# Kernel optimization log

Measured on AMD Instinct MI355X. Metric: run time of the kernel, lower is better.

Reference implementation:

```python
import jax, jax.numpy as jnp
import numpy as np

N_NODES = 50000
N_EDGES = 600000
N_GRAPHS = 64
D_NODE = 64
D_EDGE = 16
HID = 128
N_LAYERS = 3
LN_EPS = 1e-5


def setup_inputs() -> dict:
    key = jax.random.key(0)
    ks = jax.random.split(key, 16)
    inp = {
        'x': jax.random.normal(ks[0], (N_NODES, D_NODE), dtype=jnp.float32),
        'edge_index': jax.random.randint(ks[1], (2, N_EDGES), 0, N_NODES, dtype=jnp.int64),
        'edge_attr': jax.random.normal(ks[2], (N_EDGES, D_EDGE), dtype=jnp.float32),
        'batch': jnp.sort(jax.random.randint(ks[3], (N_NODES,), 0, N_GRAPHS, dtype=jnp.int64)),
    }
    def lin(k, fan_in, fan_out):
        bound = 1.0 / np.sqrt(fan_in)
        kw, kb = jax.random.split(k)
        w = jax.random.uniform(kw, (fan_in, fan_out), minval=-bound, maxval=bound, dtype=jnp.float32)
        b = jax.random.uniform(kb, (fan_out,), minval=-bound, maxval=bound, dtype=jnp.float32)
        return w, b
    inp['enc_w'], inp['enc_b'] = lin(ks[4], D_NODE, HID)
    inp['ln_g'] = jnp.ones((HID,), jnp.float32)
    inp['ln_b'] = jnp.zeros((HID,), jnp.float32)
    inp['edge_w'], inp['edge_b'] = lin(ks[5], D_EDGE, HID // 2)
    cw, cb = [], []
    for i in range(N_LAYERS):
        w, b = lin(ks[6 + i], HID, HID)
        cw.append(w); cb.append(b)
    inp['conv_ws'] = jnp.stack(cw)  # [L, HID, HID]
    inp['conv_bs'] = jnp.stack(cb)  # [L, HID]
    inp['c1_w'], inp['c1_b'] = lin(ks[10], HID, HID // 2)
    inp['c2_w'], inp['c2_b'] = lin(ks[11], HID // 2, 1)
    return inp


def _layernorm(h, g, b):
    mu = jnp.mean(h, axis=-1, keepdims=True)
    var = jnp.mean(jnp.square(h - mu), axis=-1, keepdims=True)
    return (h - mu) * jax.lax.rsqrt(var + LN_EPS) * g + b


def _gcn_forward(x, edge_attr, batch, src, dst,
                 enc_w, enc_b, ln_g, ln_b, edge_w, edge_b,
                 conv_ws, conv_bs, c1_w, c1_b, c2_w, c2_b):
    # node encoder: Linear -> ReLU -> LayerNorm
    h = _layernorm(jax.nn.relu(x @ enc_w + enc_b), ln_g, ln_b)
    # edge encoder (output unused downstream, kept for fidelity)
    _ = jax.nn.relu(edge_attr @ edge_w + edge_b)
    # GCN normalization with self-loops: deg = in-degree + 1
    deg = jax.ops.segment_sum(jnp.ones((src.shape[0],), h.dtype), dst, num_segments=N_NODES) + 1.0
    dis = jax.lax.rsqrt(deg)  # deg >= 1
    edge_norm = (dis[src] * dis[dst])[:, None]
    self_norm = (dis * dis)[:, None]  # 1/deg for self-loop
    for i in range(N_LAYERS):
        hw = h @ conv_ws[i]
        agg = jax.ops.segment_sum(hw[src] * edge_norm, dst, num_segments=N_NODES)
        h = agg + hw * self_norm + conv_bs[i]
        h = jax.nn.relu(h)  # dropout is identity at eval
    # global mean pool over graphs
    sums = jax.ops.segment_sum(h, batch, num_segments=N_GRAPHS)
    cnts = jax.ops.segment_sum(jnp.ones((h.shape[0],), h.dtype), batch, num_segments=N_GRAPHS)
    pooled = sums / jnp.maximum(cnts, 1.0)[:, None]
    # classifier: Linear -> ReLU -> (Dropout) -> Linear
    return jax.nn.relu(pooled @ c1_w + c1_b) @ c2_w + c2_b


def reference(x, edge_index, edge_attr, batch, enc_w, enc_b, ln_g, ln_b,
              edge_w, edge_b, conv_ws, conv_bs, c1_w, c1_b, c2_w, c2_b):
    src, dst = edge_index[0], edge_index[1]
    return _gcn_forward(x, edge_attr, batch, src, dst, enc_w, enc_b, ln_g, ln_b,
                        edge_w, edge_b, conv_ws, conv_bs, c1_w, c1_b, c2_w, c2_b)
```

## Files before the change

### kernel.cpp

```cpp
#include <hip/hip_runtime.h>

#define HID 128
#define DNODE 64
#define NNODES 50000
#define NEDGES 600000
#define NGRAPHS 64
#define LN_EPS 1e-5f
#define SCAN_BLK 256
#define NSCAN ((NNODES + SCAN_BLK - 1) / SCAN_BLK)

#define NZERO (NNODES + NGRAPHS * HID)
#define NZERO4 (NZERO / 4)
#define Z_BLKS ((NZERO4 + 255) / 256)
#define PKWC_BLKS (3 * 16384 / 256)
#define PKWE_BLKS (8192 / 256)

#define ENC_BLKS ((NNODES + 63) / 64)
#define CNT_BLKS ((NEDGES + 255) / 256)
#define BND_BLKS ((NNODES + 255) / 256)

#define CONV_BLKS ((NNODES + 63) / 64)
#define FILL_BLKS ((NEDGES + 255) / 256)

#define GC_BLKS (NNODES / 16)

typedef __attribute__((ext_vector_type(8))) short bf16x8;
typedef __attribute__((ext_vector_type(8))) unsigned short u16x8;
typedef __attribute__((ext_vector_type(4))) float f32x4;

static __device__ __forceinline__ unsigned short f2bf(float f) {
  unsigned int u = __float_as_uint(f);
  u += 0x7fffu + ((u >> 16) & 1u);
  return (unsigned short)(u >> 16);
}
static __device__ __forceinline__ float bf2f(unsigned short h) {
  return __uint_as_float(((unsigned int)h) << 16);
}

__global__ void __launch_bounds__(256) prep0_kernel(
    int4* __restrict__ zp, const float* __restrict__ W,
    unsigned short* __restrict__ Wp, const float* __restrict__ enc_w,
    unsigned short* __restrict__ Wpe) {
  int b = blockIdx.x;
  if (b < Z_BLKS) {
    int i = b * 256 + threadIdx.x;
    if (i < NZERO4) zp[i] = make_int4(0, 0, 0, 0);
  } else if (b < Z_BLKS + PKWC_BLKS) {
    int t = (b - Z_BLKS) * 256 + threadIdx.x;
    int i = t & 7;
    int lane = (t >> 3) & 63;
    int kk = (t >> 9) & 3;
    int nt = (t >> 11) & 7;
    int layer = t >> 14;
    int k = kk * 32 + (lane >> 4) * 8 + i;
    int n = nt * 16 + (lane & 15);
    Wp[t] = f2bf(W[((size_t)layer * HID + k) * HID + n]);
  } else {
    int t = (b - Z_BLKS - PKWC_BLKS) * 256 + threadIdx.x;
    int i = t & 7;
    int lane = (t >> 3) & 63;
    int kk = (t >> 9) & 1;
    int nt = (t >> 10) & 7;
    int k = kk * 32 + (lane >> 4) * 8 + i;
    int n = nt * 16 + (lane & 15);
    Wpe[t] = f2bf(enc_w[(size_t)k * HID + n]);
  }
}

__global__ void __launch_bounds__(256) prep1_kernel(
    const float* __restrict__ x, const unsigned short* __restrict__ Wpe,
    const float* __restrict__ enc_b, const float* __restrict__ ln_g,
    const float* __restrict__ ln_b, unsigned short* __restrict__ Abf,
    const int* __restrict__ dst, int* __restrict__ degi, int* __restrict__ erank,
    const int* __restrict__ batch, int* __restrict__ gstart,
    int* __restrict__ gend) {
  __shared__ __align__(16) unsigned short tile[4][16][136];
  int blk = blockIdx.x;
  if (blk >= ENC_BLKS) {
    int b2 = blk - ENC_BLKS;
    if (b2 < CNT_BLKS) {
      int e = b2 * 256 + threadIdx.x;
      if (e < NEDGES) erank[e] = atomicAdd(&degi[dst[e]], 1);
    } else {
      int i = (b2 - CNT_BLKS) * 256 + threadIdx.x;
      if (i < NNODES) {
        int g = batch[i];
        if (i == 0 || batch[i - 1] != g) gstart[g] = i;
        if (i == NNODES - 1 || batch[i + 1] != g) gend[g] = i + 1;
      }
    }
    return;
  }
  int wave = threadIdx.x >> 6;
  int lane = threadIdx.x & 63;
  int l15 = lane & 15, h = lane >> 4;
  int base = blk * 64 + wave * 16;
  int row = base + l15;
  int rowc = row < NNODES ? row : NNODES - 1;
  const float* xr = x + (size_t)rowc * DNODE;
  bf16x8 a[2];
#pragma unroll
  for (int kk = 0; kk < 2; ++kk) {
    float4 p0 = *(const float4*)(xr + kk * 32 + h * 8);
    float4 p1 = *(const float4*)(xr + kk * 32 + h * 8 + 4);
    a[kk][0] = (short)f2bf(p0.x); a[kk][1] = (short)f2bf(p0.y);
    a[kk][2] = (short)f2bf(p0.z); a[kk][3] = (short)f2bf(p0.w);
    a[kk][4] = (short)f2bf(p1.x); a[kk][5] = (short)f2bf(p1.y);
    a[kk][6] = (short)f2bf(p1.z); a[kk][7] = (short)f2bf(p1.w);
  }
  f32x4 acc[8];
#pragma unroll
  for (int nt = 0; nt < 8; ++nt) acc[nt] = (f32x4)(0.f);
  const bf16x8* wp = (const bf16x8*)Wpe;
#pragma unroll
  for (int kk = 0; kk < 2; ++kk)
#pragma unroll
    for (int nt = 0; nt < 8; ++nt)
      acc[nt] = __builtin_amdgcn_mfma_f32_16x16x32_bf16(a[kk], wp[(nt * 2 + kk) * 64 + lane],
                                                        acc[nt], 0, 0, 0);
  float s[4] = {0.f, 0.f, 0.f, 0.f}, s2[4] = {0.f, 0.f, 0.f, 0.f};
#pragma unroll
  for (int nt = 0; nt < 8; ++nt) {
    float bcol = enc_b[nt * 16 + l15];
#pragma unroll
    for (int r = 0; r < 4; ++r) {
      float v = fmaxf(acc[nt][r] + bcol, 0.f);
      acc[nt][r] = v;
      s[r] += v;
      s2[r] = fmaf(v, v, s2[r]);
    }
  }
#pragma unroll
  for (int r = 0; r < 4; ++r) {
#pragma unroll
    for (int o = 1; o < 16; o <<= 1) {
      s[r] += __shfl_xor(s[r], o);
      s2[r] += __shfl_xor(s2[r], o);
    }
  }
  float mu[4], rstd[4];
#pragma unroll
  for (int r = 0; r < 4; ++r) {
    mu[r] = s[r] * (1.0f / HID);
    float var = s2[r] * (1.0f / HID) - mu[r] * mu[r];
    rstd[r] = rsqrtf(var + LN_EPS);
  }
#pragma unroll
  for (int nt = 0; nt < 8; ++nt) {
    float gcol = ln_g[nt * 16 + l15], bbcol = ln_b[nt * 16 + l15];
#pragma unroll
    for (int r = 0; r < 4; ++r)
      tile[wave][h * 4 + r][nt * 16 + l15] =
          f2bf((acc[nt][r] - mu[r]) * rstd[r] * gcol + bbcol);
  }
  __syncthreads();
  int trow = lane >> 2, tseg = lane & 3;
  int orow = base + trow;
  if (orow < NNODES) {
#pragma unroll
    for (int q = 0; q < 4; ++q) {
      u16x8 v = *(const u16x8*)&tile[wave][trow][tseg * 32 + q * 8];
      *(u16x8*)(Abf + (size_t)orow * HID + tseg * 32 + q * 8) = v;
    }
  }
}

__global__ void __launch_bounds__(SCAN_BLK) blocksum_kernel(
    const int* __restrict__ degi, int* __restrict__ bsum) {
  int i = blockIdx.x * SCAN_BLK + threadIdx.x;
  int v = (i < NNODES) ? degi[i] : 0;
#pragma unroll
  for (int off = 32; off; off >>= 1) v += __shfl_down(v, off);
  __shared__ int wsum[4];
  if ((threadIdx.x & 63) == 0) wsum[threadIdx.x >> 6] = v;
  __syncthreads();
  if (threadIdx.x == 0) bsum[blockIdx.x] = wsum[0] + wsum[1] + wsum[2] + wsum[3];
}

__global__ void __launch_bounds__(SCAN_BLK) offsets_kernel(
    const int* __restrict__ degi, const int* __restrict__ bsum,
    int* __restrict__ off, float* __restrict__ dis) {
  int b = blockIdx.x, t = threadIdx.x;
  __shared__ int sb[SCAN_BLK];
  __shared__ int s[SCAN_BLK];
  __shared__ int wred[4];
  sb[t] = (t < NSCAN) ? bsum[t] : 0;
  __syncthreads();
  int v = (t < b) ? sb[t] : 0;
#pragma unroll
  for (int o = 32; o; o >>= 1) v += __shfl_down(v, o);
  if ((t & 63) == 0) wred[t >> 6] = v;
  __syncthreads();
  int base = wred[0] + wred[1] + wred[2] + wred[3];
  int i = b * SCAN_BLK + t;
  int dv = (i < NNODES) ? degi[i] : 0;
  s[t] = dv;
  __syncthreads();
  for (int d = 1; d < SCAN_BLK; d <<= 1) {
    int x = (t >= d) ? s[t - d] : 0;
    __syncthreads();
    s[t] += x;
    __syncthreads();
  }
  if (i < NNODES) {
    int excl = s[t] - dv + base;
    off[i] = excl;
    dis[i] = rsqrtf((float)dv + 1.0f);
  }
  if (b == 0 && t == 0) off[NNODES] = NEDGES;
}

__global__ void __launch_bounds__(256) fillconv_kernel(
    const unsigned short* __restrict__ Abf, const unsigned short* __restrict__ Wp,
    unsigned short* __restrict__ Bbf, const int* __restrict__ src,
    const int* __restrict__ dst, const int* __restrict__ erank,
    const int* __restrict__ off, const float* __restrict__ dis,
    int2* __restrict__ epack) {
  __shared__ __align__(16) unsigned short tile[4][16][136];
  int blk = blockIdx.x;
  if (blk >= CONV_BLKS) {
    int e = (blk - CONV_BLKS) * 256 + threadIdx.x;
    if (e >= NEDGES) return;
    int d = dst[e];
    int sN = src[e];
    int r = erank[e];
    int2 v;
    v.x = sN;
    v.y = __float_as_int(dis[sN] * dis[d]);
    epack[off[d] + r] = v;
    return;
  }
  int wave = threadIdx.x >> 6;
  int lane = threadIdx.x & 63;
  int base = blk * 64 + wave * 16;
  int l15 = lane & 15, hi = lane >> 4;
  int row = base + l15;
  int rowc = row < NNODES ? row : NNODES - 1;
  bf16x8 a[4];
#pragma unroll
  for (int kk = 0; kk < 4; ++kk)
    a[kk] = *(const bf16x8*)(Abf + (size_t)rowc * HID + kk * 32 + hi * 8);
  f32x4 acc[8];
#pragma unroll
  for (int nt = 0; nt < 8; ++nt) acc[nt] = (f32x4)(0.f);
#pragma unroll
  for (int kk = 0; kk < 4; ++kk) {
#pragma unroll
    for (int nt = 0; nt < 8; ++nt) {
      bf16x8 w = *(const bf16x8*)(Wp + (((nt * 4 + kk) * 64 + lane) << 3));
      acc[nt] = __builtin_amdgcn_mfma_f32_16x16x32_bf16(a[kk], w, acc[nt], 0, 0, 0);
    }
  }
#pragma unroll
  for (int nt = 0; nt < 8; ++nt)
#pragma unroll
    for (int r = 0; r < 4; ++r)
      tile[wave][hi * 4 + r][nt * 16 + l15] = f2bf(acc[nt][r]);
  __syncthreads();
  int trow = lane >> 2, tseg = lane & 3;
  int orow = base + trow;
  if (orow < NNODES) {
#pragma unroll
    for (int s = 0; s < 4; ++s) {
      u16x8 v = *(const u16x8*)&tile[wave][trow][tseg * 32 + s * 8];
      *(u16x8*)(Bbf + (size_t)orow * HID + tseg * 32 + s * 8) = v;
    }
  }
}

__global__ void __launch_bounds__(1024) gc_kernel(
    const int* __restrict__ off, const int2* __restrict__ epack,
    const float* __restrict__ dis, const float* __restrict__ bias,
    const unsigned short* __restrict__ Bin, const unsigned short* __restrict__ Wnext,
    unsigned short* __restrict__ Bout) {
  __shared__ __align__(16) unsigned short As[16][136];
  __shared__ __align__(16) unsigned short Bs[16][136];
  int w = threadIdx.x >> 6, lane = threadIdx.x & 63;
  int n = blockIdx.x * 16 + w;
  int slot = lane >> 4, p = lane & 15;
  int lo = off[n], hi = off[n + 1];
  float acc0[8], acc1[8];
#pragma unroll
  for (int i = 0; i < 8; ++i) { acc0[i] = 0.f; acc1[i] = 0.f; }
  int idx = lo + slot;
  for (; idx + 4 < hi; idx += 8) {
    int2 e0 = epack[idx];
    int2 e1 = epack[idx + 4];
    float w0 = __int_as_float(e0.y);
    float w1 = __int_as_float(e1.y);
    u16x8 v0 = *(const u16x8*)(Bin + (size_t)e0.x * HID + p * 8);
    u16x8 v1 = *(const u16x8*)(Bin + (size_t)e1.x * HID + p * 8);
#pragma unroll
    for (int i = 0; i < 8; ++i) acc0[i] = fmaf(bf2f(v0[i]), w0, acc0[i]);
#pragma unroll
    for (int i = 0; i < 8; ++i) acc1[i] = fmaf(bf2f(v1[i]), w1, acc1[i]);
  }
  if (idx < hi) {
    int2 e0 = epack[idx];
    float w0 = __int_as_float(e0.y);
    u16x8 v0 = *(const u16x8*)(Bin + (size_t)e0.x * HID + p * 8);
#pragma unroll
    for (int i = 0; i < 8; ++i) acc0[i] = fmaf(bf2f(v0[i]), w0, acc0[i]);
  }
#pragma unroll
  for (int i = 0; i < 8; ++i) {
    float a = acc0[i] + acc1[i];
    a += __shfl_xor(a, 16);
    a += __shfl_xor(a, 32);
    acc0[i] = a;
  }
  if (slot == 0) {
    float dn = dis[n];
    float d2 = dn * dn;
    u16x8 selfv = *(const u16x8*)(Bin + (size_t)n * HID + p * 8);
    float4 b0 = ((const float4*)bias)[p * 2];
    float4 b1 = ((const float4*)bias)[p * 2 + 1];
    float bb[8] = {b0.x, b0.y, b0.z, b0.w, b1.x, b1.y, b1.z, b1.w};
    u16x8 o;
#pragma unroll
    for (int i = 0; i < 8; ++i) {
      float v = fmaxf(fmaf(bf2f(selfv[i]), d2, bb[i]) + acc0[i], 0.f);
      o[i] = f2bf(v);
    }
    *(u16x8*)&As[w][p * 8] = o;
  }
  __syncthreads();
  if (w < 8) {
    bf16x8 a[4];
#pragma unroll
    for (int kk = 0; kk < 4; ++kk)
      a[kk] = *(const bf16x8*)&As[p][kk * 32 + slot * 8];
    f32x4 acc = (f32x4)(0.f);
#pragma unroll
    for (int kk = 0; kk < 4; ++kk) {
      bf16x8 wf = *(const bf16x8*)(Wnext + (((w * 4 + kk) * 64 + lane) << 3));
      acc = __builtin_amdgcn_mfma_f32_16x16x32_bf16(a[kk], wf, acc, 0, 0, 0);
    }
#pragma unroll
    for (int r = 0; r < 4; ++r)
      Bs[slot * 4 + r][w * 16 + p] = f2bf(acc[r]);
  }
  __syncthreads();
  if (threadIdx.x < 256) {
    int row = threadIdx.x >> 4, seg = threadIdx.x & 15;
    *(u16x8*)(Bout + (size_t)(blockIdx.x * 16 + row) * HID + seg * 8) =
        *(const u16x8*)&Bs[row][seg * 8];
  }
}

__global__ void __launch_bounds__(1024) g2pool_kernel(
    const int* __restrict__ off, const int2* __restrict__ epack,
    const float* __restrict__ dis, const float* __restrict__ bias,
    const unsigned short* __restrict__ Bin, const int* __restrict__ batch,
    float* __restrict__ sums) {
  __shared__ float Ps[16][132];
  __shared__ int bg[16];
  int w = threadIdx.x >> 6, lane = threadIdx.x & 63;
  int n = blockIdx.x * 16 + w;
  int slot = lane >> 4, p = lane & 15;
  int lo = off[n], hi = off[n + 1];
  float acc0[8], acc1[8];
#pragma unroll
  for (int i = 0; i < 8; ++i) { acc0[i] = 0.f; acc1[i] = 0.f; }
  int idx = lo + slot;
  for (; idx + 4 < hi; idx += 8) {
    int2 e0 = epack[idx];
    int2 e1 = epack[idx + 4];
    float w0 = __int_as_float(e0.y);
    float w1 = __int_as_float(e1.y);
    u16x8 v0 = *(const u16x8*)(Bin + (size_t)e0.x * HID + p * 8);
    u16x8 v1 = *(const u16x8*)(Bin + (size_t)e1.x * HID + p * 8);
#pragma unroll
    for (int i = 0; i < 8; ++i) acc0[i] = fmaf(bf2f(v0[i]), w0, acc0[i]);
#pragma unroll
    for (int i = 0; i < 8; ++i) acc1[i] = fmaf(bf2f(v1[i]), w1, acc1[i]);
  }
  if (idx < hi) {
    int2 e0 = epack[idx];
    float w0 = __int_as_float(e0.y);
    u16x8 v0 = *(const u16x8*)(Bin + (size_t)e0.x * HID + p * 8);
#pragma unroll
    for (int i = 0; i < 8; ++i) acc0[i] = fmaf(bf2f(v0[i]), w0, acc0[i]);
  }
#pragma unroll
  for (int i = 0; i < 8; ++i) {
    float a = acc0[i] + acc1[i];
    a += __shfl_xor(a, 16);
    a += __shfl_xor(a, 32);
    acc0[i] = a;
  }
  if (slot == 0) {
    float dn = dis[n];
    float d2 = dn * dn;
    u16x8 selfv = *(const u16x8*)(Bin + (size_t)n * HID + p * 8);
    float4 b0 = ((const float4*)bias)[p * 2];
    float4 b1 = ((const float4*)bias)[p * 2 + 1];
    float bb[8] = {b0.x, b0.y, b0.z, b0.w, b1.x, b1.y, b1.z, b1.w};
    float4 o0, o1;
    o0.x = fmaxf(fmaf(bf2f(selfv[0]), d2, bb[0]) + acc0[0], 0.f);
    o0.y = fmaxf(fmaf(bf2f(selfv[1]), d2, bb[1]) + acc0[1], 0.f);
    o0.z = fmaxf(fmaf(bf2f(selfv[2]), d2, bb[2]) + acc0[2], 0.f);
    o0.w = fmaxf(fmaf(bf2f(selfv[3]), d2, bb[3]) + acc0[3], 0.f);
    o1.x = fmaxf(fmaf(bf2f(selfv[4]), d2, bb[4]) + acc0[4], 0.f);
    o1.y = fmaxf(fmaf(bf2f(selfv[5]), d2, bb[5]) + acc0[5], 0.f);
    o1.z = fmaxf(fmaf(bf2f(selfv[6]), d2, bb[6]) + acc0[6], 0.f);
    o1.w = fmaxf(fmaf(bf2f(selfv[7]), d2, bb[7]) + acc0[7], 0.f);
    *(float4*)&Ps[w][p * 8] = o0;
    *(float4*)&Ps[w][p * 8 + 4] = o1;
  }
  if (threadIdx.x < 16) bg[threadIdx.x] = batch[blockIdx.x * 16 + threadIdx.x];
  __syncthreads();
  if (threadIdx.x < HID) {
    int j = threadIdx.x;
    float a = 0.f;
    int cur = bg[0];
    for (int r = 0; r < 16; ++r) {
      int g = bg[r];
      if (g != cur) { atomicAdd(&sums[cur * HID + j], a); a = 0.f; cur = g; }
      a += Ps[r][j];
    }
    atomicAdd(&sums[cur * HID + j], a);
  }
}

__global__ void __launch_bounds__(64) cls_kernel(
    const float* __restrict__ sums, const int* __restrict__ gstart,
    const int* __restrict__ gend, const float* __restrict__ c1w,
    const float* __restrict__ c1b, const float* __restrict__ c2w,
    const float* __restrict__ c2b, float* __restrict__ out) {
  int g = blockIdx.x;
  int j = threadIdx.x;
  __shared__ float pooled[HID];
  float cnt = (float)(gend[g] - gstart[g]);
  float inv = 1.0f / fmaxf(cnt, 1.0f);
  pooled[j] = sums[g * HID + j] * inv;
  pooled[j + 64] = sums[g * HID + j + 64] * inv;
  __syncthreads();
  float s = c1b[j];
#pragma unroll 8
  for (int k = 0; k < HID; ++k) s = fmaf(pooled[k], c1w[k * 64 + j], s);
  s = fmaxf(s, 0.f) * c2w[j];
#pragma unroll
  for (int off = 32; off; off >>= 1) s += __shfl_down(s, off);
  if (j == 0) out[g] = s + c2b[0];
}

extern "C" void kernel_launch(void* const* d_in, const int* in_sizes, int n_in,
                              void* d_out, int out_size, void* d_ws, size_t ws_size,
                              hipStream_t stream) {
  const float* x = (const float*)d_in[0];
  const int* edge_index = (const int*)d_in[1];
  const int* batch = (const int*)d_in[3];
  const float* enc_w = (const float*)d_in[4];
  const float* enc_b = (const float*)d_in[5];
  const float* ln_g = (const float*)d_in[6];
  const float* ln_b = (const float*)d_in[7];
  const float* conv_ws = (const float*)d_in[10];
  const float* conv_bs = (const float*)d_in[11];
  const float* c1w = (const float*)d_in[12];
  const float* c1b = (const float*)d_in[13];
  const float* c2w = (const float*)d_in[14];
  const float* c2b = (const float*)d_in[15];
  float* out = (float*)d_out;

  unsigned short* Abf = (unsigned short*)d_ws;
  unsigned short* B1 = Abf + (size_t)NNODES * HID;
  unsigned short* B2 = B1 + (size_t)NNODES * HID;
  unsigned short* Wp = B2 + (size_t)NNODES * HID;
  unsigned short* Wpe = Wp + 3 * 16384;
  int2* epack = (int2*)(Wpe + 8192);
  int* erank = (int*)(epack + NEDGES);
  int* degi = erank + NEDGES;
  float* sums = (float*)(degi + NNODES);
  int* off = (int*)(sums + NGRAPHS * HID);
  float* dis = (float*)(off + NNODES + 1);
  int* bsum = (int*)(dis + NNODES);
  int* gstart = bsum + SCAN_BLK;
  int* gend = gstart + NGRAPHS;

  const int* srcp = edge_index;
  const int* dstp = edge_index + NEDGES;

  prep0_kernel<<<Z_BLKS + PKWC_BLKS + PKWE_BLKS, 256, 0, stream>>>(
      (int4*)degi, conv_ws, Wp, enc_w, Wpe);
  prep1_kernel<<<ENC_BLKS + CNT_BLKS + BND_BLKS, 256, 0, stream>>>(
      x, Wpe, enc_b, ln_g, ln_b, Abf, dstp, degi, erank, batch, gstart, gend);
  blocksum_kernel<<<NSCAN, SCAN_BLK, 0, stream>>>(degi, bsum);
  offsets_kernel<<<NSCAN, SCAN_BLK, 0, stream>>>(degi, bsum, off, dis);
  fillconv_kernel<<<CONV_BLKS + FILL_BLKS, 256, 0, stream>>>(
      Abf, Wp, B1, srcp, dstp, erank, off, dis, epack);

  gc_kernel<<<GC_BLKS, 1024, 0, stream>>>(off, epack, dis, conv_bs, B1,
                                          Wp + (size_t)1 * 16384, B2);
  gc_kernel<<<GC_BLKS, 1024, 0, stream>>>(off, epack, dis, conv_bs + HID, B2,
                                          Wp + (size_t)2 * 16384, B1);
  g2pool_kernel<<<GC_BLKS, 1024, 0, stream>>>(off, epack, dis, conv_bs + 2 * HID,
                                              B1, batch, sums);
  cls_kernel<<<NGRAPHS, 64, 0, stream>>>(sums, gstart, gend, c1w, c1b, c2w, c2b, out);
}
```

Baseline: 183.7 us.

## Replicate degree counters to spread atomic contention in CSR build

```diff
diff --git a/kernel.cpp b/kernel.cpp
--- a/kernel.cpp
+++ b/kernel.cpp
@@ -8,16 +8,17 @@
 #define LN_EPS 1e-5f
 #define SCAN_BLK 256
 #define NSCAN ((NNODES + SCAN_BLK - 1) / SCAN_BLK)
-
-#define NZERO (NNODES + NGRAPHS * HID)
+#define NR 8
+
+#define NZERO (NR * NNODES + NGRAPHS * HID)
 #define NZERO4 (NZERO / 4)
 #define Z_BLKS ((NZERO4 + 255) / 256)
 #define PKWC_BLKS (3 * 16384 / 256)
 #define PKWE_BLKS (8192 / 256)
+#define BND_BLKS ((NNODES + 255) / 256)
 
 #define ENC_BLKS ((NNODES + 63) / 64)
-#define CNT_BLKS ((NEDGES + 255) / 256)
-#define BND_BLKS ((NNODES + 255) / 256)
+#define CNT4_BLKS ((NEDGES + 1023) / 1024)
 
 #define CONV_BLKS ((NNODES + 63) / 64)
 #define FILL_BLKS ((NEDGES + 255) / 256)
@@ -40,7 +41,8 @@
 __global__ void __launch_bounds__(256) prep0_kernel(
     int4* __restrict__ zp, const float* __restrict__ W,
     unsigned short* __restrict__ Wp, const float* __restrict__ enc_w,
-    unsigned short* __restrict__ Wpe) {
+    unsigned short* __restrict__ Wpe, const int* __restrict__ batch,
+    int* __restrict__ gstart, int* __restrict__ gend) {
   int b = blockIdx.x;
   if (b < Z_BLKS) {
     int i = b * 256 + threadIdx.x;
@@ -55,7 +57,7 @@
     int k = kk * 32 + (lane >> 4) * 8 + i;
     int n = nt * 16 + (lane & 15);
     Wp[t] = f2bf(W[((size_t)layer * HID + k) * HID + n]);
-  } else {
+  } else if (b < Z_BLKS + PKWC_BLKS + PKWE_BLKS) {
     int t = (b - Z_BLKS - PKWC_BLKS) * 256 + threadIdx.x;
     int i = t & 7;
     int lane = (t >> 3) & 63;
@@ -64,6 +66,13 @@
     int k = kk * 32 + (lane >> 4) * 8 + i;
     int n = nt * 16 + (lane & 15);
     Wpe[t] = f2bf(enc_w[(size_t)k * HID + n]);
+  } else {
+    int i = (b - Z_BLKS - PKWC_BLKS - PKWE_BLKS) * 256 + threadIdx.x;
+    if (i < NNODES) {
+      int g = batch[i];
+      if (i == 0 || batch[i - 1] != g) gstart[g] = i;
+      if (i == NNODES - 1 || batch[i + 1] != g) gend[g] = i + 1;
+    }
   }
 }
 
@@ -71,23 +80,22 @@
     const float* __restrict__ x, const unsigned short* __restrict__ Wpe,
     const float* __restrict__ enc_b, const float* __restrict__ ln_g,
     const float* __restrict__ ln_b, unsigned short* __restrict__ Abf,
-    const int* __restrict__ dst, int* __restrict__ degi, int* __restrict__ erank,
-    const int* __restrict__ batch, int* __restrict__ gstart,
-    int* __restrict__ gend) {
+    const int* __restrict__ dst, int* __restrict__ degR,
+    int* __restrict__ erank) {
   __shared__ __align__(16) unsigned short tile[4][16][136];
   int blk = blockIdx.x;
   if (blk >= ENC_BLKS) {
     int b2 = blk - ENC_BLKS;
-    if (b2 < CNT_BLKS) {
-      int e = b2 * 256 + threadIdx.x;
-      if (e < NEDGES) erank[e] = atomicAdd(&degi[dst[e]], 1);
-    } else {
-      int i = (b2 - CNT_BLKS) * 256 + threadIdx.x;
-      if (i < NNODES) {
-        int g = batch[i];
-        if (i == 0 || batch[i - 1] != g) gstart[g] = i;
-        if (i == NNODES - 1 || batch[i + 1] != g) gend[g] = i + 1;
-      }
+    int tbase = b2 * 1024 + threadIdx.x * 4;
+    if (tbase < NEDGES) {
+      int4 d4 = *(const int4*)(dst + tbase);
+      int* dr = degR + (b2 & (NR - 1)) * NNODES;
+      int4 rk;
+      rk.x = atomicAdd(&dr[d4.x], 1);
+      rk.y = atomicAdd(&dr[d4.y], 1);
+      rk.z = atomicAdd(&dr[d4.z], 1);
+      rk.w = atomicAdd(&dr[d4.w], 1);
+      *(int4*)(erank + tbase) = rk;
     }
     return;
   }
@@ -166,9 +174,19 @@
 }
 
 __global__ void __launch_bounds__(SCAN_BLK) blocksum_kernel(
-    const int* __restrict__ degi, int* __restrict__ bsum) {
+    const int* __restrict__ degR, int* __restrict__ roff,
+    int* __restrict__ degi, int* __restrict__ bsum) {
   int i = blockIdx.x * SCAN_BLK + threadIdx.x;
-  int v = (i < NNODES) ? degi[i] : 0;
+  int tot = 0;
+  if (i < NNODES) {
+#pragma unroll
+    for (int r = 0; r < NR; ++r) {
+      roff[r * NNODES + i] = tot;
+      tot += degR[r * NNODES + i];
+    }
+    degi[i] = tot;
+  }
+  int v = tot;
 #pragma unroll
   for (int off = 32; off; off >>= 1) v += __shfl_down(v, off);
   __shared__ int wsum[4];
@@ -214,8 +232,8 @@
     const unsigned short* __restrict__ Abf, const unsigned short* __restrict__ Wp,
     unsigned short* __restrict__ Bbf, const int* __restrict__ src,
     const int* __restrict__ dst, const int* __restrict__ erank,
-    const int* __restrict__ off, const float* __restrict__ dis,
-    int2* __restrict__ epack) {
+    const int* __restrict__ roff, const int* __restrict__ off,
+    const float* __restrict__ dis, int2* __restrict__ epack) {
   __shared__ __align__(16) unsigned short tile[4][16][136];
   int blk = blockIdx.x;
   if (blk >= CONV_BLKS) {
@@ -223,11 +241,12 @@
     if (e >= NEDGES) return;
     int d = dst[e];
     int sN = src[e];
-    int r = erank[e];
+    int r = (e >> 10) & (NR - 1);
+    int rank = erank[e] + roff[r * NNODES + d];
     int2 v;
     v.x = sN;
     v.y = __float_as_int(dis[sN] * dis[d]);
-    epack[off[d] + r] = v;
+    epack[off[d] + rank] = v;
     return;
   }
   int wave = threadIdx.x >> 6;
@@ -470,9 +489,11 @@
   unsigned short* Wpe = Wp + 3 * 16384;
   int2* epack = (int2*)(Wpe + 8192);
   int* erank = (int*)(epack + NEDGES);
-  int* degi = erank + NEDGES;
-  float* sums = (float*)(degi + NNODES);
-  int* off = (int*)(sums + NGRAPHS * HID);
+  int* degR = erank + NEDGES;
+  float* sums = (float*)(degR + NR * NNODES);
+  int* roff = (int*)(sums + NGRAPHS * HID);
+  int* degi = roff + NR * NNODES;
+  int* off = degi + NNODES;
   float* dis = (float*)(off + NNODES + 1);
   int* bsum = (int*)(dis + NNODES);
   int* gstart = bsum + SCAN_BLK;
@@ -481,14 +502,14 @@
   const int* srcp = edge_index;
   const int* dstp = edge_index + NEDGES;
 
-  prep0_kernel<<<Z_BLKS + PKWC_BLKS + PKWE_BLKS, 256, 0, stream>>>(
-      (int4*)degi, conv_ws, Wp, enc_w, Wpe);
-  prep1_kernel<<<ENC_BLKS + CNT_BLKS + BND_BLKS, 256, 0, stream>>>(
-      x, Wpe, enc_b, ln_g, ln_b, Abf, dstp, degi, erank, batch, gstart, gend);
-  blocksum_kernel<<<NSCAN, SCAN_BLK, 0, stream>>>(degi, bsum);
+  prep0_kernel<<<Z_BLKS + PKWC_BLKS + PKWE_BLKS + BND_BLKS, 256, 0, stream>>>(
+      (int4*)degR, conv_ws, Wp, enc_w, Wpe, batch, gstart, gend);
+  prep1_kernel<<<ENC_BLKS + CNT4_BLKS, 256, 0, stream>>>(
+      x, Wpe, enc_b, ln_g, ln_b, Abf, dstp, degR, erank);
+  blocksum_kernel<<<NSCAN, SCAN_BLK, 0, stream>>>(degR, roff, degi, bsum);
   offsets_kernel<<<NSCAN, SCAN_BLK, 0, stream>>>(degi, bsum, off, dis);
   fillconv_kernel<<<CONV_BLKS + FILL_BLKS, 256, 0, stream>>>(
-      Abf, Wp, B1, srcp, dstp, erank, off, dis, epack);
+      Abf, Wp, B1, srcp, dstp, erank, roff, off, dis, epack);
 
   gc_kernel<<<GC_BLKS, 1024, 0, stream>>>(off, epack, dis, conv_bs, B1,
                                           Wp + (size_t)1 * 16384, B2);
```

New measurement: 185.0 us. No clear change (+0.7%).

## Pack edge index and bf16 weight into one 32-bit word; reorder prep blocks

Applied to the files above, without the earlier changes.

```diff
diff --git a/kernel.cpp b/kernel.cpp
--- a/kernel.cpp
+++ b/kernel.cpp
@@ -14,10 +14,10 @@
 #define Z_BLKS ((NZERO4 + 255) / 256)
 #define PKWC_BLKS (3 * 16384 / 256)
 #define PKWE_BLKS (8192 / 256)
-
+#define BND_BLKS ((NNODES + 255) / 256)
+
+#define CNT_BLKS ((NEDGES + 255) / 256)
 #define ENC_BLKS ((NNODES + 63) / 64)
-#define CNT_BLKS ((NEDGES + 255) / 256)
-#define BND_BLKS ((NNODES + 255) / 256)
 
 #define CONV_BLKS ((NNODES + 63) / 64)
 #define FILL_BLKS ((NEDGES + 255) / 256)
@@ -40,7 +40,8 @@
 __global__ void __launch_bounds__(256) prep0_kernel(
     int4* __restrict__ zp, const float* __restrict__ W,
     unsigned short* __restrict__ Wp, const float* __restrict__ enc_w,
-    unsigned short* __restrict__ Wpe) {
+    unsigned short* __restrict__ Wpe, const int* __restrict__ batch,
+    int* __restrict__ gstart, int* __restrict__ gend) {
   int b = blockIdx.x;
   if (b < Z_BLKS) {
     int i = b * 256 + threadIdx.x;
@@ -55,7 +56,7 @@
     int k = kk * 32 + (lane >> 4) * 8 + i;
     int n = nt * 16 + (lane & 15);
     Wp[t] = f2bf(W[((size_t)layer * HID + k) * HID + n]);
-  } else {
+  } else if (b < Z_BLKS + PKWC_BLKS + PKWE_BLKS) {
     int t = (b - Z_BLKS - PKWC_BLKS) * 256 + threadIdx.x;
     int i = t & 7;
     int lane = (t >> 3) & 63;
@@ -64,6 +65,13 @@
     int k = kk * 32 + (lane >> 4) * 8 + i;
     int n = nt * 16 + (lane & 15);
     Wpe[t] = f2bf(enc_w[(size_t)k * HID + n]);
+  } else {
+    int i = (b - Z_BLKS - PKWC_BLKS - PKWE_BLKS) * 256 + threadIdx.x;
+    if (i < NNODES) {
+      int g = batch[i];
+      if (i == 0 || batch[i - 1] != g) gstart[g] = i;
+      if (i == NNODES - 1 || batch[i + 1] != g) gend[g] = i + 1;
+    }
   }
 }
 
@@ -71,30 +79,20 @@
     const float* __restrict__ x, const unsigned short* __restrict__ Wpe,
     const float* __restrict__ enc_b, const float* __restrict__ ln_g,
     const float* __restrict__ ln_b, unsigned short* __restrict__ Abf,
-    const int* __restrict__ dst, int* __restrict__ degi, int* __restrict__ erank,
-    const int* __restrict__ batch, int* __restrict__ gstart,
-    int* __restrict__ gend) {
+    const int* __restrict__ dst, int* __restrict__ degi,
+    int* __restrict__ erank) {
   __shared__ __align__(16) unsigned short tile[4][16][136];
   int blk = blockIdx.x;
-  if (blk >= ENC_BLKS) {
-    int b2 = blk - ENC_BLKS;
-    if (b2 < CNT_BLKS) {
-      int e = b2 * 256 + threadIdx.x;
-      if (e < NEDGES) erank[e] = atomicAdd(&degi[dst[e]], 1);
-    } else {
-      int i = (b2 - CNT_BLKS) * 256 + threadIdx.x;
-      if (i < NNODES) {
-        int g = batch[i];
-        if (i == 0 || batch[i - 1] != g) gstart[g] = i;
-        if (i == NNODES - 1 || batch[i + 1] != g) gend[g] = i + 1;
-      }
-    }
+  if (blk < CNT_BLKS) {
+    int e = blk * 256 + threadIdx.x;
+    if (e < NEDGES) erank[e] = atomicAdd(&degi[dst[e]], 1);
     return;
   }
+  int b2 = blk - CNT_BLKS;
   int wave = threadIdx.x >> 6;
   int lane = threadIdx.x & 63;
   int l15 = lane & 15, h = lane >> 4;
-  int base = blk * 64 + wave * 16;
+  int base = b2 * 64 + wave * 16;
   int row = base + l15;
   int rowc = row < NNODES ? row : NNODES - 1;
   const float* xr = x + (size_t)rowc * DNODE;
@@ -215,7 +213,7 @@
     unsigned short* __restrict__ Bbf, const int* __restrict__ src,
     const int* __restrict__ dst, const int* __restrict__ erank,
     const int* __restrict__ off, const float* __restrict__ dis,
-    int2* __restrict__ epack) {
+    unsigned int* __restrict__ epack) {
   __shared__ __align__(16) unsigned short tile[4][16][136];
   int blk = blockIdx.x;
   if (blk >= CONV_BLKS) {
@@ -224,10 +222,8 @@
     int d = dst[e];
     int sN = src[e];
     int r = erank[e];
-    int2 v;
-    v.x = sN;
-    v.y = __float_as_int(dis[sN] * dis[d]);
-    epack[off[d] + r] = v;
+    epack[off[d] + r] =
+        ((unsigned int)f2bf(dis[sN] * dis[d]) << 16) | (unsigned int)sN;
     return;
   }
   int wave = threadIdx.x >> 6;
@@ -269,7 +265,7 @@
 }
 
 __global__ void __launch_bounds__(1024) gc_kernel(
-    const int* __restrict__ off, const int2* __restrict__ epack,
+    const int* __restrict__ off, const unsigned int* __restrict__ epack,
     const float* __restrict__ dis, const float* __restrict__ bias,
     const unsigned short* __restrict__ Bin, const unsigned short* __restrict__ Wnext,
     unsigned short* __restrict__ Bout) {
@@ -284,21 +280,21 @@
   for (int i = 0; i < 8; ++i) { acc0[i] = 0.f; acc1[i] = 0.f; }
   int idx = lo + slot;
   for (; idx + 4 < hi; idx += 8) {
-    int2 e0 = epack[idx];
-    int2 e1 = epack[idx + 4];
-    float w0 = __int_as_float(e0.y);
-    float w1 = __int_as_float(e1.y);
-    u16x8 v0 = *(const u16x8*)(Bin + (size_t)e0.x * HID + p * 8);
-    u16x8 v1 = *(const u16x8*)(Bin + (size_t)e1.x * HID + p * 8);
+    unsigned int e0 = epack[idx];
+    unsigned int e1 = epack[idx + 4];
+    float w0 = bf2f((unsigned short)(e0 >> 16));
+    float w1 = bf2f((unsigned short)(e1 >> 16));
+    u16x8 v0 = *(const u16x8*)(Bin + (size_t)(e0 & 0xFFFFu) * HID + p * 8);
+    u16x8 v1 = *(const u16x8*)(Bin + (size_t)(e1 & 0xFFFFu) * HID + p * 8);
 #pragma unroll
     for (int i = 0; i < 8; ++i) acc0[i] = fmaf(bf2f(v0[i]), w0, acc0[i]);
 #pragma unroll
     for (int i = 0; i < 8; ++i) acc1[i] = fmaf(bf2f(v1[i]), w1, acc1[i]);
   }
   if (idx < hi) {
-    int2 e0 = epack[idx];
-    float w0 = __int_as_float(e0.y);
-    u16x8 v0 = *(const u16x8*)(Bin + (size_t)e0.x * HID + p * 8);
+    unsigned int e0 = epack[idx];
+    float w0 = bf2f((unsigned short)(e0 >> 16));
+    u16x8 v0 = *(const u16x8*)(Bin + (size_t)(e0 & 0xFFFFu) * HID + p * 8);
 #pragma unroll
     for (int i = 0; i < 8; ++i) acc0[i] = fmaf(bf2f(v0[i]), w0, acc0[i]);
   }
@@ -349,7 +345,7 @@
 }
 
 __global__ void __launch_bounds__(1024) g2pool_kernel(
-    const int* __restrict__ off, const int2* __restrict__ epack,
+    const int* __restrict__ off, const unsigned int* __restrict__ epack,
     const float* __restrict__ dis, const float* __restrict__ bias,
     const unsigned short* __restrict__ Bin, const int* __restrict__ batch,
     float* __restrict__ sums) {
@@ -364,21 +360,21 @@
   for (int i = 0; i < 8; ++i) { acc0[i] = 0.f; acc1[i] = 0.f; }
   int idx = lo + slot;
   for (; idx + 4 < hi; idx += 8) {
-    int2 e0 = epack[idx];
-    int2 e1 = epack[idx + 4];
-    float w0 = __int_as_float(e0.y);
-    float w1 = __int_as_float(e1.y);
-    u16x8 v0 = *(const u16x8*)(Bin + (size_t)e0.x * HID + p * 8);
-    u16x8 v1 = *(const u16x8*)(Bin + (size_t)e1.x * HID + p * 8);
+    unsigned int e0 = epack[idx];
+    unsigned int e1 = epack[idx + 4];
+    float w0 = bf2f((unsigned short)(e0 >> 16));
+    float w1 = bf2f((unsigned short)(e1 >> 16));
+    u16x8 v0 = *(const u16x8*)(Bin + (size_t)(e0 & 0xFFFFu) * HID + p * 8);
+    u16x8 v1 = *(const u16x8*)(Bin + (size_t)(e1 & 0xFFFFu) * HID + p * 8);
 #pragma unroll
     for (int i = 0; i < 8; ++i) acc0[i] = fmaf(bf2f(v0[i]), w0, acc0[i]);
 #pragma unroll
     for (int i = 0; i < 8; ++i) acc1[i] = fmaf(bf2f(v1[i]), w1, acc1[i]);
   }
   if (idx < hi) {
-    int2 e0 = epack[idx];
-    float w0 = __int_as_float(e0.y);
-    u16x8 v0 = *(const u16x8*)(Bin + (size_t)e0.x * HID + p * 8);
+    unsigned int e0 = epack[idx];
+    float w0 = bf2f((unsigned short)(e0 >> 16));
+    u16x8 v0 = *(const u16x8*)(Bin + (size_t)(e0 & 0xFFFFu) * HID + p * 8);
 #pragma unroll
     for (int i = 0; i < 8; ++i) acc0[i] = fmaf(bf2f(v0[i]), w0, acc0[i]);
   }
@@ -468,7 +464,7 @@
   unsigned short* B2 = B1 + (size_t)NNODES * HID;
   unsigned short* Wp = B2 + (size_t)NNODES * HID;
   unsigned short* Wpe = Wp + 3 * 16384;
-  int2* epack = (int2*)(Wpe + 8192);
+  unsigned int* epack = (unsigned int*)(Wpe + 8192);
   int* erank = (int*)(epack + NEDGES);
   int* degi = erank + NEDGES;
   float* sums = (float*)(degi + NNODES);
@@ -481,10 +477,10 @@
   const int* srcp = edge_index;
   const int* dstp = edge_index + NEDGES;
 
-  prep0_kernel<<<Z_BLKS + PKWC_BLKS + PKWE_BLKS, 256, 0, stream>>>(
-      (int4*)degi, conv_ws, Wp, enc_w, Wpe);
-  prep1_kernel<<<ENC_BLKS + CNT_BLKS + BND_BLKS, 256, 0, stream>>>(
-      x, Wpe, enc_b, ln_g, ln_b, Abf, dstp, degi, erank, batch, gstart, gend);
+  prep0_kernel<<<Z_BLKS + PKWC_BLKS + PKWE_BLKS + BND_BLKS, 256, 0, stream>>>(
+      (int4*)degi, conv_ws, Wp, enc_w, Wpe, batch, gstart, gend);
+  prep1_kernel<<<CNT_BLKS + ENC_BLKS, 256, 0, stream>>>(
+      x, Wpe, enc_b, ln_g, ln_b, Abf, dstp, degi, erank);
   blocksum_kernel<<<NSCAN, SCAN_BLK, 0, stream>>>(degi, bsum);
   offsets_kernel<<<NSCAN, SCAN_BLK, 0, stream>>>(degi, bsum, off, dis);
   fillconv_kernel<<<CONV_BLKS + FILL_BLKS, 256, 0, stream>>>(
```

New measurement: 182.5 us. No clear change (-0.7%).
